# Kernel optimization log

Hardware: AMD Instinct MI355X
Metric: run time of the kernel (lower is better)

The kernel has to match this reference:

```python
import jax, jax.numpy as jnp
import numpy as np

N_NODES = 100000
N_EDGES = 20000
NNZ = 1600000


def _hconv(x, node_idx, edge_idx, W, b):
    # PyG HypergraphConv (no attention): out = D^-1 H (B^-1 H^T (x W)) + b
    xw = x @ W  # [N, F_out]
    ones = jnp.ones((node_idx.shape[0],), dtype=x.dtype)
    Bdeg = jax.ops.segment_sum(ones, edge_idx, num_segments=N_EDGES)
    Binv = jnp.where(Bdeg > 0, 1.0 / Bdeg, 0.0)
    # node -> hyperedge aggregation
    e = jax.ops.segment_sum(xw[node_idx], edge_idx, num_segments=N_EDGES)
    e = e * Binv[:, None]
    Ddeg = jax.ops.segment_sum(ones, node_idx, num_segments=N_NODES)
    Dinv = jnp.where(Ddeg > 0, 1.0 / Ddeg, 0.0)
    # hyperedge -> node aggregation
    out = jax.ops.segment_sum(e[edge_idx], node_idx, num_segments=N_NODES)
    return out * Dinv[:, None] + b


def setup_inputs() -> dict:
    key = jax.random.key(0)
    ks = jax.random.split(key, 12)
    x = jax.random.normal(ks[0], (N_NODES, 300), dtype=jnp.float32)
    node_idx = jax.random.randint(ks[1], (NNZ,), 0, N_NODES)
    edge_idx = jax.random.randint(ks[2], (NNZ,), 0, N_EDGES)
    hyper_edge_index = jnp.stack([node_idx, edge_idx], axis=0)
    def lin(kw, kb, fi, fo):
        s = 1.0 / np.sqrt(fi)
        W = jax.random.uniform(kw, (fi, fo), jnp.float32, -s, s)
        b = jax.random.uniform(kb, (fo,), jnp.float32, -s, s)
        return W, b
    W1, b1 = lin(ks[3], ks[4], 300, 256)
    W2, b2 = lin(ks[5], ks[6], 256, 256)
    W3, b3 = lin(ks[7], ks[8], 256, 128)
    attn_W, attn_b = lin(ks[9], ks[10], 128, 1)
    return {"x": x, "hyper_edge_index": hyper_edge_index,
            "W1": W1, "b1": b1, "W2": W2, "b2": b2,
            "W3": W3, "b3": b3, "attn_W": attn_W, "attn_b": attn_b}


def reference(x, hyper_edge_index, W1, b1, W2, b2, W3, b3, attn_W, attn_b):
    node_idx = hyper_edge_index[0]
    edge_idx = hyper_edge_index[1]
    h = jax.nn.leaky_relu(_hconv(x, node_idx, edge_idx, W1, b1), negative_slope=0.01)
    # dropout is identity at inference
    h = jax.nn.leaky_relu(_hconv(h, node_idx, edge_idx, W2, b2), negative_slope=0.01)
    h = _hconv(h, node_idx, edge_idx, W3, b3)  # [N, 128]
    # attention pooling over all nodes (softmax along dim 0)
    logits = h @ attn_W + attn_b  # [N, 1]
    attn = jax.nn.softmax(logits, axis=0)
    return jnp.sum(attn * h, axis=0)  # [128]
```

## Files before the change

kernel.cpp:

```cpp
#include <hip/hip_runtime.h>
#include <hip/hip_bf16.h>
#include <string.h>

#define N_NODES 100000
#define N_EDGES 20000
#define NNZ     1600000

#define CHUNK   8192
#define NBE     157
#define NBN     391
#define CAP_E   11264
#define CAP_N   4864
#define NBLK_BIN ((NNZ + CHUNK - 1) / CHUNK)


__device__ __forceinline__ unsigned short f2bf(float f) {
    unsigned int u = __float_as_uint(f);
    unsigned int r = (u + 0x7fffu + ((u >> 16) & 1u)) >> 16;
    return (unsigned short)r;
}
__device__ __forceinline__ float bflo(unsigned int v) { return __uint_as_float(v << 16); }
__device__ __forceinline__ float bfhi(unsigned int v) { return __uint_as_float(v & 0xffff0000u); }
__device__ __forceinline__ unsigned int packbf(float lo, float hi) {
    return ((unsigned int)f2bf(hi) << 16) | (unsigned int)f2bf(lo);
}

__device__ __forceinline__ void async_copy16(const void* g, void* l) {
    __builtin_amdgcn_global_load_lds((const __attribute__((address_space(1))) void*)g,
                                     (__attribute__((address_space(3))) void*)l, 16, 0, 0);
}

typedef __attribute__((ext_vector_type(8))) short bf16x8;
typedef __attribute__((ext_vector_type(4))) float f32x4;


__global__ __launch_bounds__(256)
void bin_both(const int* __restrict__ node_idx, const int* __restrict__ edge_idx,
              int* __restrict__ curE, int* __restrict__ curN,
              unsigned int* __restrict__ stagedE, unsigned int* __restrict__ stagedN) {
    __shared__ int hE[NBE], gE[NBE], hN[NBN], gN[NBN];
    int t = threadIdx.x;
    for (int i = t; i < NBE; i += 256) hE[i] = 0;
    for (int i = t; i < NBN; i += 256) hN[i] = 0;
    __syncthreads();
    long base = (long)blockIdx.x * CHUNK;
    for (int k = 0; k < CHUNK / 256; k++) {
        long i = base + t + k * 256;
        if (i < NNZ) {
            atomicAdd(&hE[edge_idx[i] >> 7], 1);
            atomicAdd(&hN[node_idx[i] >> 8], 1);
        }
    }
    __syncthreads();
    for (int i = t; i < NBE; i += 256) gE[i] = hE[i] ? atomicAdd(&curE[i], hE[i]) : 0;
    for (int i = t; i < NBN; i += 256) gN[i] = hN[i] ? atomicAdd(&curN[i], hN[i]) : 0;
    __syncthreads();
    for (int i = t; i < NBE; i += 256) hE[i] = 0;
    for (int i = t; i < NBN; i += 256) hN[i] = 0;
    __syncthreads();
    for (int k = 0; k < CHUNK / 256; k++) {
        long i = base + t + k * 256;
        if (i < NNZ) {
            int e = edge_idx[i], n = node_idx[i];
            int be = e >> 7, bn = n >> 8;
            int pe = gE[be] + atomicAdd(&hE[be], 1);
            if (pe < CAP_E) stagedE[(size_t)be * CAP_E + pe] = ((unsigned)e << 17) | (unsigned)n;
            int pn = gN[bn] + atomicAdd(&hN[bn], 1);
            if (pn < CAP_N) stagedN[(size_t)bn * CAP_N + pn] = ((unsigned)n << 15) | (unsigned)e;
        }
    }
}

__global__ __launch_bounds__(256)
void build_csr2(const unsigned int* __restrict__ staged, const int* __restrict__ cnts,
                int cap, int kshift, int bshift, int nkey,
                int* __restrict__ off, int* __restrict__ endv,
                float* __restrict__ inv, int* __restrict__ csr) {
    __shared__ int cnt[256];
    __shared__ int cur[256];
    int b = blockIdx.x, t = threadIdx.x;
    int kpb = 1 << bshift;
    int key0 = b << bshift;
    unsigned int vmask = (1u << kshift) - 1u;
    int s = b * cap;
    int n = min(cnts[b], cap);
    if (t < kpb) cnt[t] = 0;
    __syncthreads();
    for (int j = t; j < n; j += 256)
        atomicAdd(&cnt[(int)(staged[s + j] >> kshift) - key0], 1);
    __syncthreads();
    int v = (t < kpb) ? cnt[t] : 0;
    cur[t] = v; __syncthreads();
    for (int st = 1; st < 256; st <<= 1) {
        int x = (t >= st) ? cur[t - st] : 0;
        __syncthreads();
        cur[t] += x;
        __syncthreads();
    }
    int excl = cur[t] - v;
    __syncthreads();
    if (t < kpb) {
        int key = key0 + t;
        if (key < nkey) {
            off[key] = s + excl;
            endv[key] = s + excl + v;
            inv[key] = (v > 0) ? 1.0f / (float)v : 0.0f;
        }
        cur[t] = excl;
    }
    __syncthreads();
    for (int j = t; j < n; j += 256) {
        unsigned int pk = staged[s + j];
        int k = (int)(pk >> kshift) - key0;
        int pos = s + atomicAdd(&cur[k], 1);
        csr[pos] = (int)(pk & vmask);
    }
}


__global__ void convert_pad_x(const float* __restrict__ x, unsigned short* __restrict__ xb) {
    int idx = blockIdx.x * 256 + threadIdx.x;
    if (idx < N_NODES * 320) {
        int r = idx / 320, k = idx - r * 320;
        xb[idx] = (k < 300) ? f2bf(x[(size_t)r * 300 + k]) : (unsigned short)0;
    }
}

__global__ void transpose_all(const float* __restrict__ W1, const float* __restrict__ W2,
                              const float* __restrict__ W3,
                              unsigned short* __restrict__ Wt1, unsigned short* __restrict__ Wt2,
                              unsigned short* __restrict__ Wt3) {
    int b = blockIdx.x;
    int t = threadIdx.x;
    if (b < 256) {
        for (int k = t; k < 320; k += 256)
            Wt1[(size_t)b * 320 + k] = (k < 300) ? f2bf(W1[(size_t)k * 256 + b]) : (unsigned short)0;
    } else if (b < 512) {
        int n = b - 256;
        Wt2[(size_t)n * 256 + t] = f2bf(W2[(size_t)t * 256 + n]);
    } else {
        int n = b - 512;
        Wt3[(size_t)n * 256 + t] = f2bf(W3[(size_t)t * 128 + n]);
    }
}


__global__ __launch_bounds__(256)
void gemm_bf16(const unsigned short* __restrict__ A,
               const unsigned short* __restrict__ Bt,
               unsigned short* __restrict__ C,
               int M, int Kp, int N) {
    __shared__ unsigned short As[128 * 32];
    __shared__ unsigned short Bs[128 * 32];
    int tid = threadIdx.x;
    int lane = tid & 63;
    int w = tid >> 6;
    int row0 = blockIdx.x * 128;
    int col0 = blockIdx.y * 128;
    int wm = w & 1, wn = w >> 1;

    f32x4 acc[4][4];
    #pragma unroll
    for (int i = 0; i < 4; i++)
        #pragma unroll
        for (int j = 0; j < 4; j++) acc[i][j] = (f32x4){0.f, 0.f, 0.f, 0.f};

    int sr = lane >> 2;
    int sc = lane & 3;

    for (int k0 = 0; k0 < Kp; k0 += 32) {
        #pragma unroll
        for (int c = 0; c < 2; c++) {
            int r = w * 32 + c * 16 + sr;
            int gr = row0 + r; if (gr >= M) gr = M - 1;
            const unsigned short* g = A + (size_t)gr * Kp + k0 + sc * 8;
            async_copy16(g, (void*)(As + (w * 32 + c * 16) * 32));
        }
        #pragma unroll
        for (int c = 0; c < 2; c++) {
            int r = w * 32 + c * 16 + sr;
            const unsigned short* g = Bt + (size_t)(col0 + r) * Kp + k0 + sc * 8;
            async_copy16(g, (void*)(Bs + (w * 32 + c * 16) * 32));
        }
        __syncthreads();

        bf16x8 a[4], b[4];
        #pragma unroll
        for (int i = 0; i < 4; i++)
            a[i] = *(const bf16x8*)(As + (wm * 64 + i * 16 + (lane & 15)) * 32 + (lane >> 4) * 8);
        #pragma unroll
        for (int j = 0; j < 4; j++)
            b[j] = *(const bf16x8*)(Bs + (wn * 64 + j * 16 + (lane & 15)) * 32 + (lane >> 4) * 8);
        #pragma unroll
        for (int i = 0; i < 4; i++)
            #pragma unroll
            for (int j = 0; j < 4; j++)
                acc[i][j] = __builtin_amdgcn_mfma_f32_16x16x32_bf16(a[i], b[j], acc[i][j], 0, 0, 0);
        __syncthreads();
    }

    int crow = (lane >> 4) * 4;
    int ccol = lane & 15;
    #pragma unroll
    for (int i = 0; i < 4; i++)
        #pragma unroll
        for (int r = 0; r < 4; r++) {
            int gr = row0 + wm * 64 + i * 16 + crow + r;
            if (gr < M) {
                #pragma unroll
                for (int j = 0; j < 4; j++) {
                    int gc = col0 + wn * 64 + j * 16 + ccol;
                    C[(size_t)gr * N + gc] = f2bf(acc[i][j][r]);
                }
            }
        }
}


#define ACC8(v)  { a[0] += bflo((v).x); a[1] += bfhi((v).x); \
                   a[2] += bflo((v).y); a[3] += bfhi((v).y); \
                   a[4] += bflo((v).z); a[5] += bfhi((v).z); \
                   a[6] += bflo((v).w); a[7] += bfhi((v).w); }

__global__ __launch_bounds__(256)
void edge_agg256(const unsigned short* __restrict__ X, const int* __restrict__ off,
                 const int* __restrict__ endv, const int* __restrict__ csr,
                 const float* __restrict__ inv, unsigned short* __restrict__ E) {
    int wv = threadIdx.x >> 6, lane = threadIdx.x & 63;
    int seg = blockIdx.x * 4 + wv;
    if (seg >= N_EDGES) return;
    int s = off[seg], t = endv[seg];
    int half = lane >> 5, l32 = lane & 31;
    const uint4* Xp = (const uint4*)X;
    float a[8] = {0.f, 0.f, 0.f, 0.f, 0.f, 0.f, 0.f, 0.f};
    int j = s;
    for (; j + 8 <= t; j += 8) {
        uint4 v[4];
        #pragma unroll
        for (int q = 0; q < 4; q++) v[q] = Xp[(size_t)csr[j + 2 * q + half] * 32 + l32];
        #pragma unroll
        for (int q = 0; q < 4; q++) ACC8(v[q]);
    }
    for (; j + 1 < t; j += 2) {
        uint4 v = Xp[(size_t)csr[j + half] * 32 + l32];
        ACC8(v);
    }
    if (j < t && half == 0) {
        uint4 v = Xp[(size_t)csr[j] * 32 + l32];
        ACC8(v);
    }
    #pragma unroll
    for (int k = 0; k < 8; k++) a[k] += __shfl_down(a[k], 32);
    if (half == 0) {
        float bi = inv[seg];
        uint4 o;
        o.x = packbf(a[0] * bi, a[1] * bi); o.y = packbf(a[2] * bi, a[3] * bi);
        o.z = packbf(a[4] * bi, a[5] * bi); o.w = packbf(a[6] * bi, a[7] * bi);
        ((uint4*)E)[(size_t)seg * 32 + l32] = o;
    }
}

__global__ __launch_bounds__(256)
void node_agg256(const unsigned short* __restrict__ Eb, const int* __restrict__ off,
                 const int* __restrict__ endv, const int* __restrict__ csr,
                 const float* __restrict__ inv, const float* __restrict__ bias,
                 unsigned short* __restrict__ outB) {
    int wv = threadIdx.x >> 6, lane = threadIdx.x & 63;
    int seg = blockIdx.x * 4 + wv;
    if (seg >= N_NODES) return;
    int s = off[seg], t = endv[seg];
    int half = lane >> 5, l32 = lane & 31;
    const uint4* Ep = (const uint4*)Eb;
    float a[8] = {0.f, 0.f, 0.f, 0.f, 0.f, 0.f, 0.f, 0.f};
    int j = s;
    for (; j + 8 <= t; j += 8) {
        uint4 v[4];
        #pragma unroll
        for (int q = 0; q < 4; q++) v[q] = Ep[(size_t)csr[j + 2 * q + half] * 32 + l32];
        #pragma unroll
        for (int q = 0; q < 4; q++) ACC8(v[q]);
    }
    for (; j + 1 < t; j += 2) {
        uint4 v = Ep[(size_t)csr[j + half] * 32 + l32];
        ACC8(v);
    }
    if (j < t && half == 0) {
        uint4 v = Ep[(size_t)csr[j] * 32 + l32];
        ACC8(v);
    }
    #pragma unroll
    for (int k = 0; k < 8; k++) a[k] += __shfl_down(a[k], 32);
    if (half == 0) {
        float di = inv[seg];
        float4 b0 = ((const float4*)bias)[l32 * 2];
        float4 b1 = ((const float4*)bias)[l32 * 2 + 1];
        float o0 = a[0] * di + b0.x, o1 = a[1] * di + b0.y;
        float o2 = a[2] * di + b0.z, o3 = a[3] * di + b0.w;
        float o4 = a[4] * di + b1.x, o5 = a[5] * di + b1.y;
        float o6 = a[6] * di + b1.z, o7 = a[7] * di + b1.w;
        o0 = (o0 > 0.f) ? o0 : 0.01f * o0;  o1 = (o1 > 0.f) ? o1 : 0.01f * o1;
        o2 = (o2 > 0.f) ? o2 : 0.01f * o2;  o3 = (o3 > 0.f) ? o3 : 0.01f * o3;
        o4 = (o4 > 0.f) ? o4 : 0.01f * o4;  o5 = (o5 > 0.f) ? o5 : 0.01f * o5;
        o6 = (o6 > 0.f) ? o6 : 0.01f * o6;  o7 = (o7 > 0.f) ? o7 : 0.01f * o7;
        uint4 o;
        o.x = packbf(o0, o1); o.y = packbf(o2, o3);
        o.z = packbf(o4, o5); o.w = packbf(o6, o7);
        ((uint4*)outB)[(size_t)seg * 32 + l32] = o;
    }
}

__global__ __launch_bounds__(256)
void node_agg128f(const unsigned short* __restrict__ Eb, const int* __restrict__ off,
                  const int* __restrict__ endv, const int* __restrict__ csr,
                  const float* __restrict__ inv, const float* __restrict__ bias,
                  float* __restrict__ outF) {
    int wv = threadIdx.x >> 6, lane = threadIdx.x & 63;
    int seg = blockIdx.x * 4 + wv;
    if (seg >= N_NODES) return;
    int s = off[seg], t = endv[seg];
    int quad = lane >> 4, l16 = lane & 15;
    const uint4* Ep = (const uint4*)Eb;
    float a[8] = {0.f, 0.f, 0.f, 0.f, 0.f, 0.f, 0.f, 0.f};
    int j = s;
    for (; j + 8 <= t; j += 8) {
        uint4 v0 = Ep[(size_t)csr[j + quad] * 16 + l16];
        uint4 v1 = Ep[(size_t)csr[j + 4 + quad] * 16 + l16];
        ACC8(v0); ACC8(v1);
    }
    for (; j + 4 <= t; j += 4) {
        uint4 v = Ep[(size_t)csr[j + quad] * 16 + l16];
        ACC8(v);
    }
    if (j < t && j + quad < t) {
        uint4 v = Ep[(size_t)csr[j + quad] * 16 + l16];
        ACC8(v);
    }
    #pragma unroll
    for (int k = 0; k < 8; k++) {
        a[k] += __shfl_down(a[k], 32);
        a[k] += __shfl_down(a[k], 16);
    }
    if (lane < 16) {
        float di = inv[seg];
        float4 b0 = ((const float4*)bias)[l16 * 2];
        float4 b1 = ((const float4*)bias)[l16 * 2 + 1];
        float4 o0 = make_float4(a[0] * di + b0.x, a[1] * di + b0.y,
                                a[2] * di + b0.z, a[3] * di + b0.w);
        float4 o1 = make_float4(a[4] * di + b1.x, a[5] * di + b1.y,
                                a[6] * di + b1.z, a[7] * di + b1.w);
        ((float4*)outF)[(size_t)seg * 32 + l16 * 2]     = o0;
        ((float4*)outF)[(size_t)seg * 32 + l16 * 2 + 1] = o1;
    }
}


__global__ __launch_bounds__(256)
void logits_kernel(const float* __restrict__ H, const float* __restrict__ aW,
                   const float* __restrict__ aB, float* __restrict__ logits,
                   float* __restrict__ pmax, int N) {
    int lane = threadIdx.x & 63;
    int wave = threadIdx.x >> 6;
    int waveGlobal = blockIdx.x * 4 + wave;
    int stride = gridDim.x * 4;
    float2 w2 = ((const float2*)aW)[lane];
    float lmax = -1e30f;
    float ab = aB[0];
    for (int n = waveGlobal; n < N; n += stride) {
        float2 h2 = ((const float2*)(H + (size_t)n * 128))[lane];
        float d = h2.x * w2.x + h2.y * w2.y;
        #pragma unroll
        for (int s = 32; s > 0; s >>= 1) d += __shfl_xor(d, s, 64);
        float lg = d + ab;
        if (lane == 0) logits[n] = lg;
        lmax = fmaxf(lmax, lg);
    }
    __shared__ float wmax[4];
    if (lane == 0) wmax[wave] = lmax;
    __syncthreads();
    if (threadIdx.x == 0) {
        float m = fmaxf(fmaxf(wmax[0], wmax[1]), fmaxf(wmax[2], wmax[3]));
        pmax[blockIdx.x] = m;
    }
}

__global__ __launch_bounds__(256)
void reduce_max(const float* __restrict__ pmax, int n, float* __restrict__ gmax) {
    __shared__ float sm[256];
    float m = -1e30f;
    for (int i = threadIdx.x; i < n; i += 256) m = fmaxf(m, pmax[i]);
    sm[threadIdx.x] = m;
    __syncthreads();
    for (int s = 128; s > 0; s >>= 1) {
        if (threadIdx.x < (unsigned)s) sm[threadIdx.x] = fmaxf(sm[threadIdx.x], sm[threadIdx.x + s]);
        __syncthreads();
    }
    if (threadIdx.x == 0) *gmax = sm[0];
}

__global__ __launch_bounds__(128)
void weighted_sum(const float* __restrict__ H, const float* __restrict__ logits,
                  const float* __restrict__ gmax, float* __restrict__ gacc,
                  float* __restrict__ gsum, int N) {
    int f = threadIdx.x;
    float mx = *gmax;
    float acc = 0.f, ls = 0.f;
    for (int n = blockIdx.x; n < N; n += gridDim.x) {
        float w = __expf(logits[n] - mx);
        acc += w * H[(size_t)n * 128 + f];
        if (f == 0) ls += w;
    }
    atomicAdd(&gacc[f], acc);
    if (f == 0) atomicAdd(gsum, ls);
}

__global__ __launch_bounds__(128)
void finalize(const float* __restrict__ gacc, const float* __restrict__ gsum,
              float* __restrict__ out) {
    int f = threadIdx.x;
    out[f] = gacc[f] / gsum[0];
}


extern "C" void kernel_launch(void* const* d_in, const int* in_sizes, int n_in,
                              void* d_out, int out_size, void* d_ws, size_t ws_size,
                              hipStream_t stream) {
    const float* x        = (const float*)d_in[0];
    const int*   node_idx = (const int*)d_in[1];
    const int*   edge_idx = node_idx + NNZ;
    const float* W1 = (const float*)d_in[2];
    const float* b1 = (const float*)d_in[3];
    const float* W2 = (const float*)d_in[4];
    const float* b2 = (const float*)d_in[5];
    const float* W3 = (const float*)d_in[6];
    const float* b3 = (const float*)d_in[7];
    const float* aW = (const float*)d_in[8];
    const float* aB = (const float*)d_in[9];
    float* out = (float*)d_out;

    char* ws = (char*)d_ws;
    size_t off = 0;
    auto take = [&](size_t bytes) -> char* {
        char* r = ws + off;
        off = (off + bytes + 255) & ~(size_t)255;
        return r;
    };

    char* cur_base = take((size_t)(NBE + NBN) * 4);
    int* curE = (int*)cur_base;
    int* curN = curE + NBE;
    int*   offE = (int*)take((size_t)N_EDGES * 4);
    int*   endE = (int*)take((size_t)N_EDGES * 4);
    int*   offN = (int*)take((size_t)N_NODES * 4);
    int*   endN = (int*)take((size_t)N_NODES * 4);
    float* Binv = (float*)take((size_t)N_EDGES * 4);
    float* Dinv = (float*)take((size_t)N_NODES * 4);
    int*   csrE = (int*)take((size_t)NBE * CAP_E * 4);
    int*   csrN = (int*)take((size_t)NBN * CAP_N * 4);

    unsigned short* xb  = (unsigned short*)take((size_t)N_NODES * 320 * 2);
    unsigned short* Wt1 = (unsigned short*)take((size_t)256 * 320 * 2);
    unsigned short* Wt2 = (unsigned short*)take((size_t)256 * 256 * 2);
    unsigned short* Wt3 = (unsigned short*)take((size_t)128 * 256 * 2);
    unsigned short* xw   = (unsigned short*)take((size_t)N_NODES * 256 * 2);
    unsigned short* hb   = (unsigned short*)take((size_t)N_NODES * 256 * 2);
    unsigned short* eagg = (unsigned short*)take((size_t)N_EDGES * 256 * 2);
    unsigned short* eb   = (unsigned short*)take((size_t)N_EDGES * 256 * 2);
    float* h3 = (float*)xb;

    unsigned int* stagedE = (unsigned int*)xw;
    unsigned int* stagedN = stagedE + (size_t)NBE * CAP_E;

    float* logits = (float*)take((size_t)N_NODES * 4);
    float* pmax   = (float*)take(400 * 4);
    char* acc_base = take((128 + 1) * 4);
    float* gacc = (float*)acc_base;
    float* gsum = gacc + 128;
    float* gmax = (float*)take(4);

    hipMemsetAsync(cur_base, 0, (size_t)(NBE + NBN) * 4, stream);
    hipMemsetAsync(acc_base, 0, (128 + 1) * 4, stream);

    bin_both<<<NBLK_BIN, 256, 0, stream>>>(node_idx, edge_idx, curE, curN, stagedE, stagedN);
    build_csr2<<<NBE, 256, 0, stream>>>(stagedE, curE, CAP_E, 17, 7, N_EDGES, offE, endE, Binv, csrE);
    build_csr2<<<NBN, 256, 0, stream>>>(stagedN, curN, CAP_N, 15, 8, N_NODES, offN, endN, Dinv, csrN);

    convert_pad_x<<<(N_NODES * 320 + 255) / 256, 256, 0, stream>>>(x, xb);
    transpose_all<<<640, 256, 0, stream>>>(W1, W2, W3, Wt1, Wt2, Wt3);

    const int MB = (N_NODES + 127) / 128;
    const int ME = (N_EDGES + 127) / 128;
    const int EB = N_EDGES / 4;
    const int NB = N_NODES / 4;

    gemm_bf16<<<dim3(MB, 2), 256, 0, stream>>>(xb, Wt1, xw, N_NODES, 320, 256);
    edge_agg256<<<EB, 256, 0, stream>>>(xw, offE, endE, csrE, Binv, eb);
    node_agg256<<<NB, 256, 0, stream>>>(eb, offN, endN, csrN, Dinv, b1, hb);

    edge_agg256<<<EB, 256, 0, stream>>>(hb, offE, endE, csrE, Binv, eagg);
    gemm_bf16<<<dim3(ME, 2), 256, 0, stream>>>(eagg, Wt2, eb, N_EDGES, 256, 256);
    node_agg256<<<NB, 256, 0, stream>>>(eb, offN, endN, csrN, Dinv, b2, hb);

    edge_agg256<<<EB, 256, 0, stream>>>(hb, offE, endE, csrE, Binv, eagg);
    gemm_bf16<<<dim3(ME, 1), 256, 0, stream>>>(eagg, Wt3, eb, N_EDGES, 256, 128);
    node_agg128f<<<NB, 256, 0, stream>>>(eb, offN, endN, csrN, Dinv, b3, h3);

    logits_kernel<<<400, 256, 0, stream>>>(h3, aW, aB, logits, pmax, N_NODES);
    reduce_max<<<1, 256, 0, stream>>>(pmax, 400, gmax);
    weighted_sum<<<512, 128, 0, stream>>>(h3, logits, gmax, gacc, gsum, N_NODES);
    finalize<<<1, 128, 0, stream>>>(gacc, gsum, out);
}
```

Measured before the change: 1.023 ms.

## Slice gather-aggregation kernels by feature column and vectorize input conversion

Edge and node aggregation kernels now split the 256-wide feature row into eight 64-byte column slices, each handled by separate blocks. Within a wave, 16 rows are gathered in parallel with 4 lanes per row, followed by a shuffle reduction. This is meant to raise memory-level parallelism and shrink each block's working set in cache, at the cost of rereading the CSR indices once per slice. Other changes: index loads become nontemporal, x conversion uses vectorized 8-element packing, and the max reduction is folded into weighted_sum, which removes one launch.

```diff
diff --git a/kernel.cpp b/kernel.cpp
--- a/kernel.cpp
+++ b/kernel.cpp
@@ -32,6 +32,10 @@
 
 typedef __attribute__((ext_vector_type(8))) short bf16x8;
 typedef __attribute__((ext_vector_type(4))) float f32x4;
+
+__device__ __forceinline__ int ntload_i(const int* p) {
+    return __builtin_nontemporal_load(p);
+}
 
 
 __global__ __launch_bounds__(256)
@@ -118,12 +122,28 @@
 }
 
 
-__global__ void convert_pad_x(const float* __restrict__ x, unsigned short* __restrict__ xb) {
-    int idx = blockIdx.x * 256 + threadIdx.x;
-    if (idx < N_NODES * 320) {
-        int r = idx / 320, k = idx - r * 320;
-        xb[idx] = (k < 300) ? f2bf(x[(size_t)r * 300 + k]) : (unsigned short)0;
-    }
+__global__ __launch_bounds__(256)
+void convert_pad_x_v(const float* __restrict__ x, unsigned short* __restrict__ xb) {
+    int t = threadIdx.x;
+    if (t >= 240) return;
+    int c = t % 40;
+    int r = blockIdx.x * 6 + t / 40;
+    if (r >= N_NODES) return;
+    const float* xr = x + (size_t)r * 300 + c * 8;
+    uint4 ov;
+    if (c < 37) {
+        float4 a = ((const float4*)xr)[0];
+        float4 b = ((const float4*)xr)[1];
+        ov.x = packbf(a.x, a.y); ov.y = packbf(a.z, a.w);
+        ov.z = packbf(b.x, b.y); ov.w = packbf(b.z, b.w);
+    } else if (c == 37) {
+        float4 a = ((const float4*)xr)[0];
+        ov.x = packbf(a.x, a.y); ov.y = packbf(a.z, a.w);
+        ov.z = 0u; ov.w = 0u;
+    } else {
+        ov.x = ov.y = ov.z = ov.w = 0u;
+    }
+    *(uint4*)(xb + (size_t)r * 320 + c * 8) = ov;
 }
 
 __global__ void transpose_all(const float* __restrict__ W1, const float* __restrict__ W2,
@@ -222,134 +242,152 @@
                    a[4] += bflo((v).z); a[5] += bfhi((v).z); \
                    a[6] += bflo((v).w); a[7] += bfhi((v).w); }
 
-__global__ __launch_bounds__(256)
-void edge_agg256(const unsigned short* __restrict__ X, const int* __restrict__ off,
+#define RED16()  _Pragma("unroll") \
+                 for (int k = 0; k < 8; k++) { \
+                     a[k] += __shfl_down(a[k], 32); \
+                     a[k] += __shfl_down(a[k], 16); \
+                     a[k] += __shfl_down(a[k], 8); \
+                     a[k] += __shfl_down(a[k], 4); \
+                 }
+
+__global__ __launch_bounds__(256)
+void edge_agg_sl(const unsigned short* __restrict__ X, const int* __restrict__ off,
                  const int* __restrict__ endv, const int* __restrict__ csr,
                  const float* __restrict__ inv, unsigned short* __restrict__ E) {
     int wv = threadIdx.x >> 6, lane = threadIdx.x & 63;
-    int seg = blockIdx.x * 4 + wv;
-    if (seg >= N_EDGES) return;
-    int s = off[seg], t = endv[seg];
-    int half = lane >> 5, l32 = lane & 31;
-    const uint4* Xp = (const uint4*)X;
-    float a[8] = {0.f, 0.f, 0.f, 0.f, 0.f, 0.f, 0.f, 0.f};
-    int j = s;
-    for (; j + 8 <= t; j += 8) {
-        uint4 v[4];
-        #pragma unroll
-        for (int q = 0; q < 4; q++) v[q] = Xp[(size_t)csr[j + 2 * q + half] * 32 + l32];
-        #pragma unroll
-        for (int q = 0; q < 4; q++) ACC8(v[q]);
-    }
-    for (; j + 1 < t; j += 2) {
-        uint4 v = Xp[(size_t)csr[j + half] * 32 + l32];
-        ACC8(v);
-    }
-    if (j < t && half == 0) {
-        uint4 v = Xp[(size_t)csr[j] * 32 + l32];
-        ACC8(v);
-    }
-    #pragma unroll
-    for (int k = 0; k < 8; k++) a[k] += __shfl_down(a[k], 32);
-    if (half == 0) {
-        float bi = inv[seg];
-        uint4 o;
-        o.x = packbf(a[0] * bi, a[1] * bi); o.y = packbf(a[2] * bi, a[3] * bi);
-        o.z = packbf(a[4] * bi, a[5] * bi); o.w = packbf(a[6] * bi, a[7] * bi);
-        ((uint4*)E)[(size_t)seg * 32 + l32] = o;
-    }
-}
-
-__global__ __launch_bounds__(256)
-void node_agg256(const unsigned short* __restrict__ Eb, const int* __restrict__ off,
+    int slice = blockIdx.x & 7;
+    int seg0 = (blockIdx.x >> 3) * 16 + wv * 4;
+    int sub = lane & 3, rq = lane >> 2;
+    unsigned lo = ((unsigned)slice << 6) + ((unsigned)sub << 4);
+    const char* Xc = (const char*)X;
+    #pragma unroll 1
+    for (int ss = 0; ss < 4; ss++) {
+        int seg = seg0 + ss;
+        if (seg >= N_EDGES) break;
+        int s = off[seg], t = endv[seg];
+        float a[8] = {0.f, 0.f, 0.f, 0.f, 0.f, 0.f, 0.f, 0.f};
+        int j = s;
+        for (; j + 64 <= t; j += 64) {
+            uint4 v[4];
+            #pragma unroll
+            for (int q = 0; q < 4; q++) {
+                unsigned idx = (unsigned)ntload_i(&csr[j + q * 16 + rq]);
+                v[q] = *(const uint4*)(Xc + ((idx << 9) + lo));
+            }
+            __builtin_amdgcn_sched_barrier(0);
+            #pragma unroll
+            for (int q = 0; q < 4; q++) ACC8(v[q]);
+        }
+        for (; j + 16 <= t; j += 16) {
+            unsigned idx = (unsigned)ntload_i(&csr[j + rq]);
+            uint4 v = *(const uint4*)(Xc + ((idx << 9) + lo));
+            ACC8(v);
+        }
+        if (j + rq < t) {
+            unsigned idx = (unsigned)ntload_i(&csr[j + rq]);
+            uint4 v = *(const uint4*)(Xc + ((idx << 9) + lo));
+            ACC8(v);
+        }
+        RED16();
+        if (lane < 4) {
+            float bi = inv[seg];
+            uint4 o;
+            o.x = packbf(a[0] * bi, a[1] * bi); o.y = packbf(a[2] * bi, a[3] * bi);
+            o.z = packbf(a[4] * bi, a[5] * bi); o.w = packbf(a[6] * bi, a[7] * bi);
+            *(uint4*)((char*)E + (size_t)seg * 512 + lo) = o;
+        }
+    }
+}
+
+__global__ __launch_bounds__(256)
+void node_agg_sl(const unsigned short* __restrict__ Eb, const int* __restrict__ off,
                  const int* __restrict__ endv, const int* __restrict__ csr,
                  const float* __restrict__ inv, const float* __restrict__ bias,
                  unsigned short* __restrict__ outB) {
     int wv = threadIdx.x >> 6, lane = threadIdx.x & 63;
-    int seg = blockIdx.x * 4 + wv;
-    if (seg >= N_NODES) return;
-    int s = off[seg], t = endv[seg];
-    int half = lane >> 5, l32 = lane & 31;
-    const uint4* Ep = (const uint4*)Eb;
-    float a[8] = {0.f, 0.f, 0.f, 0.f, 0.f, 0.f, 0.f, 0.f};
-    int j = s;
-    for (; j + 8 <= t; j += 8) {
-        uint4 v[4];
-        #pragma unroll
-        for (int q = 0; q < 4; q++) v[q] = Ep[(size_t)csr[j + 2 * q + half] * 32 + l32];
-        #pragma unroll
-        for (int q = 0; q < 4; q++) ACC8(v[q]);
-    }
-    for (; j + 1 < t; j += 2) {
-        uint4 v = Ep[(size_t)csr[j + half] * 32 + l32];
-        ACC8(v);
-    }
-    if (j < t && half == 0) {
-        uint4 v = Ep[(size_t)csr[j] * 32 + l32];
-        ACC8(v);
-    }
-    #pragma unroll
-    for (int k = 0; k < 8; k++) a[k] += __shfl_down(a[k], 32);
-    if (half == 0) {
-        float di = inv[seg];
-        float4 b0 = ((const float4*)bias)[l32 * 2];
-        float4 b1 = ((const float4*)bias)[l32 * 2 + 1];
-        float o0 = a[0] * di + b0.x, o1 = a[1] * di + b0.y;
-        float o2 = a[2] * di + b0.z, o3 = a[3] * di + b0.w;
-        float o4 = a[4] * di + b1.x, o5 = a[5] * di + b1.y;
-        float o6 = a[6] * di + b1.z, o7 = a[7] * di + b1.w;
-        o0 = (o0 > 0.f) ? o0 : 0.01f * o0;  o1 = (o1 > 0.f) ? o1 : 0.01f * o1;
-        o2 = (o2 > 0.f) ? o2 : 0.01f * o2;  o3 = (o3 > 0.f) ? o3 : 0.01f * o3;
-        o4 = (o4 > 0.f) ? o4 : 0.01f * o4;  o5 = (o5 > 0.f) ? o5 : 0.01f * o5;
-        o6 = (o6 > 0.f) ? o6 : 0.01f * o6;  o7 = (o7 > 0.f) ? o7 : 0.01f * o7;
-        uint4 o;
-        o.x = packbf(o0, o1); o.y = packbf(o2, o3);
-        o.z = packbf(o4, o5); o.w = packbf(o6, o7);
-        ((uint4*)outB)[(size_t)seg * 32 + l32] = o;
-    }
-}
-
-__global__ __launch_bounds__(256)
-void node_agg128f(const unsigned short* __restrict__ Eb, const int* __restrict__ off,
-                  const int* __restrict__ endv, const int* __restrict__ csr,
-                  const float* __restrict__ inv, const float* __restrict__ bias,
-                  float* __restrict__ outF) {
+    int slice = blockIdx.x & 7;
+    int seg0 = (blockIdx.x >> 3) * 32 + wv * 8;
+    int sub = lane & 3, rq = lane >> 2;
+    unsigned lo = ((unsigned)slice << 6) + ((unsigned)sub << 4);
+    const char* Ec = (const char*)Eb;
+    float4 b0 = ((const float4*)bias)[slice * 8 + sub * 2];
+    float4 b1 = ((const float4*)bias)[slice * 8 + sub * 2 + 1];
+    #pragma unroll 1
+    for (int ss = 0; ss < 8; ss++) {
+        int seg = seg0 + ss;
+        if (seg >= N_NODES) break;
+        int s = off[seg], t = endv[seg];
+        float a[8] = {0.f, 0.f, 0.f, 0.f, 0.f, 0.f, 0.f, 0.f};
+        int j = s;
+        for (; j + 16 <= t; j += 16) {
+            unsigned idx = (unsigned)ntload_i(&csr[j + rq]);
+            uint4 v = *(const uint4*)(Ec + ((idx << 9) + lo));
+            ACC8(v);
+        }
+        if (j + rq < t) {
+            unsigned idx = (unsigned)ntload_i(&csr[j + rq]);
+            uint4 v = *(const uint4*)(Ec + ((idx << 9) + lo));
+            ACC8(v);
+        }
+        RED16();
+        if (lane < 4) {
+            float di = inv[seg];
+            float o0 = a[0] * di + b0.x, o1 = a[1] * di + b0.y;
+            float o2 = a[2] * di + b0.z, o3 = a[3] * di + b0.w;
+            float o4 = a[4] * di + b1.x, o5 = a[5] * di + b1.y;
+            float o6 = a[6] * di + b1.z, o7 = a[7] * di + b1.w;
+            o0 = (o0 > 0.f) ? o0 : 0.01f * o0;  o1 = (o1 > 0.f) ? o1 : 0.01f * o1;
+            o2 = (o2 > 0.f) ? o2 : 0.01f * o2;  o3 = (o3 > 0.f) ? o3 : 0.01f * o3;
+            o4 = (o4 > 0.f) ? o4 : 0.01f * o4;  o5 = (o5 > 0.f) ? o5 : 0.01f * o5;
+            o6 = (o6 > 0.f) ? o6 : 0.01f * o6;  o7 = (o7 > 0.f) ? o7 : 0.01f * o7;
+            uint4 o;
+            o.x = packbf(o0, o1); o.y = packbf(o2, o3);
+            o.z = packbf(o4, o5); o.w = packbf(o6, o7);
+            *(uint4*)((char*)outB + (size_t)seg * 512 + lo) = o;
+        }
+    }
+}
+
+__global__ __launch_bounds__(256)
+void node_agg128f_sl(const unsigned short* __restrict__ Eb, const int* __restrict__ off,
+                     const int* __restrict__ endv, const int* __restrict__ csr,
+                     const float* __restrict__ inv, const float* __restrict__ bias,
+                     float* __restrict__ outF) {
     int wv = threadIdx.x >> 6, lane = threadIdx.x & 63;
-    int seg = blockIdx.x * 4 + wv;
-    if (seg >= N_NODES) return;
-    int s = off[seg], t = endv[seg];
-    int quad = lane >> 4, l16 = lane & 15;
-    const uint4* Ep = (const uint4*)Eb;
-    float a[8] = {0.f, 0.f, 0.f, 0.f, 0.f, 0.f, 0.f, 0.f};
-    int j = s;
-    for (; j + 8 <= t; j += 8) {
-        uint4 v0 = Ep[(size_t)csr[j + quad] * 16 + l16];
-        uint4 v1 = Ep[(size_t)csr[j + 4 + quad] * 16 + l16];
-        ACC8(v0); ACC8(v1);
-    }
-    for (; j + 4 <= t; j += 4) {
-        uint4 v = Ep[(size_t)csr[j + quad] * 16 + l16];
-        ACC8(v);
-    }
-    if (j < t && j + quad < t) {
-        uint4 v = Ep[(size_t)csr[j + quad] * 16 + l16];
-        ACC8(v);
-    }
-    #pragma unroll
-    for (int k = 0; k < 8; k++) {
-        a[k] += __shfl_down(a[k], 32);
-        a[k] += __shfl_down(a[k], 16);
-    }
-    if (lane < 16) {
-        float di = inv[seg];
-        float4 b0 = ((const float4*)bias)[l16 * 2];
-        float4 b1 = ((const float4*)bias)[l16 * 2 + 1];
-        float4 o0 = make_float4(a[0] * di + b0.x, a[1] * di + b0.y,
-                                a[2] * di + b0.z, a[3] * di + b0.w);
-        float4 o1 = make_float4(a[4] * di + b1.x, a[5] * di + b1.y,
-                                a[6] * di + b1.z, a[7] * di + b1.w);
-        ((float4*)outF)[(size_t)seg * 32 + l16 * 2]     = o0;
-        ((float4*)outF)[(size_t)seg * 32 + l16 * 2 + 1] = o1;
+    int slice = blockIdx.x & 3;
+    int seg0 = (blockIdx.x >> 2) * 32 + wv * 8;
+    int sub = lane & 3, rq = lane >> 2;
+    unsigned lo = ((unsigned)slice << 6) + ((unsigned)sub << 4);
+    const char* Ec = (const char*)Eb;
+    float4 b0 = ((const float4*)bias)[slice * 8 + sub * 2];
+    float4 b1 = ((const float4*)bias)[slice * 8 + sub * 2 + 1];
+    #pragma unroll 1
+    for (int ss = 0; ss < 8; ss++) {
+        int seg = seg0 + ss;
+        if (seg >= N_NODES) break;
+        int s = off[seg], t = endv[seg];
+        float a[8] = {0.f, 0.f, 0.f, 0.f, 0.f, 0.f, 0.f, 0.f};
+        int j = s;
+        for (; j + 16 <= t; j += 16) {
+            unsigned idx = (unsigned)ntload_i(&csr[j + rq]);
+            uint4 v = *(const uint4*)(Ec + ((idx << 8) + lo));
+            ACC8(v);
+        }
+        if (j + rq < t) {
+            unsigned idx = (unsigned)ntload_i(&csr[j + rq]);
+            uint4 v = *(const uint4*)(Ec + ((idx << 8) + lo));
+            ACC8(v);
+        }
+        RED16();
+        if (lane < 4) {
+            float di = inv[seg];
+            float4 o0 = make_float4(a[0] * di + b0.x, a[1] * di + b0.y,
+                                    a[2] * di + b0.z, a[3] * di + b0.w);
+            float4 o1 = make_float4(a[4] * di + b1.x, a[5] * di + b1.y,
+                                    a[6] * di + b1.z, a[7] * di + b1.w);
+            ((float4*)outF)[(size_t)seg * 32 + slice * 8 + sub * 2]     = o0;
+            ((float4*)outF)[(size_t)seg * 32 + slice * 8 + sub * 2 + 1] = o1;
+        }
     }
 }
 
@@ -383,26 +421,19 @@
     }
 }
 
-__global__ __launch_bounds__(256)
-void reduce_max(const float* __restrict__ pmax, int n, float* __restrict__ gmax) {
-    __shared__ float sm[256];
-    float m = -1e30f;
-    for (int i = threadIdx.x; i < n; i += 256) m = fmaxf(m, pmax[i]);
-    sm[threadIdx.x] = m;
-    __syncthreads();
-    for (int s = 128; s > 0; s >>= 1) {
-        if (threadIdx.x < (unsigned)s) sm[threadIdx.x] = fmaxf(sm[threadIdx.x], sm[threadIdx.x + s]);
-        __syncthreads();
-    }
-    if (threadIdx.x == 0) *gmax = sm[0];
-}
-
 __global__ __launch_bounds__(128)
 void weighted_sum(const float* __restrict__ H, const float* __restrict__ logits,
-                  const float* __restrict__ gmax, float* __restrict__ gacc,
+                  const float* __restrict__ pmax, float* __restrict__ gacc,
                   float* __restrict__ gsum, int N) {
     int f = threadIdx.x;
-    float mx = *gmax;
+    __shared__ float smax[2];
+    float m = -1e30f;
+    for (int i = f; i < 400; i += 128) m = fmaxf(m, pmax[i]);
+    #pragma unroll
+    for (int s = 32; s > 0; s >>= 1) m = fmaxf(m, __shfl_xor(m, s, 64));
+    if ((f & 63) == 0) smax[f >> 6] = m;
+    __syncthreads();
+    float mx = fmaxf(smax[0], smax[1]);
     float acc = 0.f, ls = 0.f;
     for (int n = blockIdx.x; n < N; n += gridDim.x) {
         float w = __expf(logits[n] - mx);
@@ -475,7 +506,6 @@
     char* acc_base = take((128 + 1) * 4);
     float* gacc = (float*)acc_base;
     float* gsum = gacc + 128;
-    float* gmax = (float*)take(4);
 
     hipMemsetAsync(cur_base, 0, (size_t)(NBE + NBN) * 4, stream);
     hipMemsetAsync(acc_base, 0, (128 + 1) * 4, stream);
@@ -484,28 +514,28 @@
     build_csr2<<<NBE, 256, 0, stream>>>(stagedE, curE, CAP_E, 17, 7, N_EDGES, offE, endE, Binv, csrE);
     build_csr2<<<NBN, 256, 0, stream>>>(stagedN, curN, CAP_N, 15, 8, N_NODES, offN, endN, Dinv, csrN);
 
-    convert_pad_x<<<(N_NODES * 320 + 255) / 256, 256, 0, stream>>>(x, xb);
+    convert_pad_x_v<<<(N_NODES + 5) / 6, 256, 0, stream>>>(x, xb);
     transpose_all<<<640, 256, 0, stream>>>(W1, W2, W3, Wt1, Wt2, Wt3);
 
     const int MB = (N_NODES + 127) / 128;
     const int ME = (N_EDGES + 127) / 128;
-    const int EB = N_EDGES / 4;
-    const int NB = N_NODES / 4;
+    const int GE = (N_EDGES / 16) * 8;
+    const int GN = (N_NODES / 32) * 8;
+    const int GF = (N_NODES / 32) * 4;
 
     gemm_bf16<<<dim3(MB, 2), 256, 0, stream>>>(xb, Wt1, xw, N_NODES, 320, 256);
-    edge_agg256<<<EB, 256, 0, stream>>>(xw, offE, endE, csrE, Binv, eb);
-    node_agg256<<<NB, 256, 0, stream>>>(eb, offN, endN, csrN, Dinv, b1, hb);
-
-    edge_agg256<<<EB, 256, 0, stream>>>(hb, offE, endE, csrE, Binv, eagg);
+    edge_agg_sl<<<GE, 256, 0, stream>>>(xw, offE, endE, csrE, Binv, eb);
+    node_agg_sl<<<GN, 256, 0, stream>>>(eb, offN, endN, csrN, Dinv, b1, hb);
+
+    edge_agg_sl<<<GE, 256, 0, stream>>>(hb, offE, endE, csrE, Binv, eagg);
     gemm_bf16<<<dim3(ME, 2), 256, 0, stream>>>(eagg, Wt2, eb, N_EDGES, 256, 256);
-    node_agg256<<<NB, 256, 0, stream>>>(eb, offN, endN, csrN, Dinv, b2, hb);
-
-    edge_agg256<<<EB, 256, 0, stream>>>(hb, offE, endE, csrE, Binv, eagg);
+    node_agg_sl<<<GN, 256, 0, stream>>>(eb, offN, endN, csrN, Dinv, b2, hb);
+
+    edge_agg_sl<<<GE, 256, 0, stream>>>(hb, offE, endE, csrE, Binv, eagg);
     gemm_bf16<<<dim3(ME, 1), 256, 0, stream>>>(eagg, Wt3, eb, N_EDGES, 256, 128);
-    node_agg128f<<<NB, 256, 0, stream>>>(eb, offN, endN, csrN, Dinv, b3, h3);
+    node_agg128f_sl<<<GF, 256, 0, stream>>>(eb, offN, endN, csrN, Dinv, b3, h3);
 
     logits_kernel<<<400, 256, 0, stream>>>(h3, aW, aB, logits, pmax, N_NODES);
-    reduce_max<<<1, 256, 0, stream>>>(pmax, 400, gmax);
-    weighted_sum<<<512, 128, 0, stream>>>(h3, logits, gmax, gacc, gsum, N_NODES);
+    weighted_sum<<<512, 128, 0, stream>>>(h3, logits, pmax, gacc, gsum, N_NODES);
     finalize<<<1, 128, 0, stream>>>(gacc, gsum, out);
 }
```

After: 1.769 ms. 1.73x slower.
